# Kernel optimization log

Measured on AMD Instinct MI355X. Metric: run time of the kernel, lower is better.

## Reference

```python
import jax, jax.numpy as jnp
import numpy as np
from itertools import permutations

B, S, D = 1024, 16, 128
G_DIMS = [256, 256]
F_DIMS = [256, 256]

# all ordered pairs (i, j), i != j, in the same lexicographic order as
# itertools.permutations used by the torch module
_PAIRS = np.array(list(permutations(range(S), 2)), dtype=np.int32)  # [P, 2], P = S*(S-1)


def _init_linear(key, in_dim, out_dim):
    kw, kb = jax.random.split(key)
    bound = 1.0 / np.sqrt(in_dim)
    W = jax.random.uniform(kw, (in_dim, out_dim), jnp.float32, -bound, bound)
    b = jax.random.uniform(kb, (out_dim,), jnp.float32, -bound, bound)
    return W, b


def setup_inputs() -> dict:
    key = jax.random.key(0)
    ks = jax.random.split(key, 5)
    state = jax.random.normal(ks[0], (B, S, D), jnp.float32)
    gW0, gb0 = _init_linear(ks[1], 2 * D, G_DIMS[0])
    gW1, gb1 = _init_linear(ks[2], G_DIMS[0], G_DIMS[1])
    fW0, fb0 = _init_linear(ks[3], G_DIMS[1], F_DIMS[0])
    fW1, fb1 = _init_linear(ks[4], F_DIMS[0], F_DIMS[1])
    return {"state": state,
            "gW0": gW0, "gb0": gb0, "gW1": gW1, "gb1": gb1,
            "fW0": fW0, "fb0": fb0, "fW1": fW1, "fb1": fb1}


def reference(state, gW0, gb0, gW1, gb1, fW0, fb0, fW1, fb1):
    i_idx = jnp.asarray(_PAIRS[:, 0])
    j_idx = jnp.asarray(_PAIRS[:, 1])
    # gather + concat all ordered pairs: [B, P, 2D]
    paired = jnp.concatenate([state[:, i_idx], state[:, j_idx]], axis=-1)
    # g-MLP applied per pair
    h = jax.nn.relu(jnp.einsum('bpd,de->bpe', paired, gW0) + gb0)
    h = jax.nn.relu(jnp.einsum('bpd,de->bpe', h, gW1) + gb1)
    # sum over pairs -> [B, g_out]
    pooled = h.sum(axis=1)
    # f-MLP
    out = jax.nn.relu(pooled @ fW0 + fb0)
    out = jax.nn.relu(out @ fW1 + fb1)
    return out
```

## Files before the change

### kernel.cpp

```cpp
#include <hip/hip_runtime.h>

typedef __attribute__((ext_vector_type(8))) _Float16 f16x8;
typedef __attribute__((ext_vector_type(4))) float f32x4;

#define HSTR 264

__global__ __launch_bounds__(256) void prep_kernel(
    const float* __restrict__ gW0, const float* __restrict__ gW1,
    _Float16* __restrict__ W0c, _Float16* __restrict__ W1c)
{
  const int t = blockIdx.x * 256 + threadIdx.x;
  {
    const int c = t >> 7, k = t & 127;
    const int dst = ((k >> 5) * 32 + (c >> 4)) * 512 +
                    (((k >> 3) & 3) * 16 + (c & 15)) * 8 + (k & 7);
    const int src = (k + ((c >= 256) ? 128 : 0)) * 256 + (c & 255);
    W0c[dst] = (_Float16)gW0[src];
  }
  {
    const int n = t >> 8, k = t & 255;
    const int dst = ((k >> 5) * 16 + (n >> 4)) * 512 +
                    (((k >> 3) & 3) * 16 + (n & 15)) * 8 + (k & 7);
    W1c[dst] = (_Float16)gW1[k * 256 + n];
  }
}

__global__ __launch_bounds__(512, 4) void pair_kernel(
    const float* __restrict__ state,
    const _Float16* __restrict__ W0c, const float* __restrict__ gb0,
    const _Float16* __restrict__ W1c, const float* __restrict__ gb1,
    float* __restrict__ pooled)
{
  const int b   = blockIdx.x;
  const int tid = threadIdx.x;
  const int w   = tid >> 6;
  const int l   = tid & 63;
  const int lr  = l & 15;
  const int lg  = l >> 4;

  __shared__ _Float16 A_lds[16 * HSTR];
  __shared__ _Float16 C_lds[16 * HSTR];

  const float* stb = state + (size_t)b * 2048;

  f16x8 sfrag[4];
  #pragma unroll
  for (int kk = 0; kk < 4; ++kk) {
    const float* sp = stb + lr * 128 + kk * 32 + lg * 8;
    f32x4 s0 = *(const f32x4*)sp;
    f32x4 s1 = *(const f32x4*)(sp + 4);
    f16x8 f;
    f[0] = (_Float16)s0[0]; f[1] = (_Float16)s0[1];
    f[2] = (_Float16)s0[2]; f[3] = (_Float16)s0[3];
    f[4] = (_Float16)s1[0]; f[5] = (_Float16)s1[1];
    f[6] = (_Float16)s1[2]; f[7] = (_Float16)s1[3];
    sfrag[kk] = f;
  }

  const f32x4 z4 = {0.f, 0.f, 0.f, 0.f};
  f32x4 acc2[4];
  #pragma unroll
  for (int nt = 0; nt < 4; ++nt) acc2[nt] = z4;

  #pragma unroll
  for (int nt = 0; nt < 4; ++nt) {
    #pragma unroll
    for (int kk = 0; kk < 4; ++kk) {
      f16x8 bf = *(const f16x8*)(W0c + (size_t)((kk * 32 + 4 * w + nt) * 512 + l * 8));
      acc2[nt] = __builtin_amdgcn_mfma_f32_16x16x32_f16(sfrag[kk], bf, acc2[nt], 0, 0, 0);
    }
  }

  #pragma unroll
  for (int nt = 0; nt < 4; ++nt) {
    const int col = 64 * w + 16 * nt + lr;
    #pragma unroll
    for (int r = 0; r < 4; ++r) {
      const int row = lg * 4 + r;
      const float v = acc2[nt][r];
      if (col < 256) A_lds[row * HSTR + col]       = (_Float16)(v + gb0[col]);
      else           C_lds[row * HSTR + col - 256] = (_Float16)v;
    }
  }

  f16x8 bw[2][8];
  #pragma unroll
  for (int nt = 0; nt < 2; ++nt) {
    #pragma unroll
    for (int kk = 0; kk < 8; ++kk) {
      bw[nt][kk] = *(const f16x8*)(W1c + (size_t)((kk * 16 + 2 * w + nt) * 512 + l * 8));
      asm volatile("" : "+a"(bw[nt][kk]));
    }
  }

  float gb1v[2];
  #pragma unroll
  for (int nt = 0; nt < 2; ++nt) gb1v[nt] = gb1[32 * w + 16 * nt + lr];

  __syncthreads();

  f16x8 creg[8];
  #pragma unroll
  for (int kk = 0; kk < 8; ++kk)
    creg[kk] = *(const f16x8*)&C_lds[lr * HSTR + kk * 32 + lg * 8];

  const f16x8 zh = {(_Float16)0, (_Float16)0, (_Float16)0, (_Float16)0,
                    (_Float16)0, (_Float16)0, (_Float16)0, (_Float16)0};

  float pp[2] = {0.f, 0.f};
  #pragma unroll 1
  for (int i = 0; i < 16; ++i) {
    f32x4 a0 = z4, a1 = z4;
    #pragma unroll
    for (int kk = 0; kk < 8; ++kk) {
      f16x8 av = *(const f16x8*)&A_lds[i * HSTR + kk * 32 + lg * 8];
      f16x8 u = __builtin_elementwise_max(av + creg[kk], zh);
      asm volatile("s_nop 3\n\tv_mfma_f32_16x16x32_f16 %0, %1, %2, %0"
                   : "+v"(a0) : "v"(u), "a"(bw[0][kk]));
      asm volatile("v_mfma_f32_16x16x32_f16 %0, %1, %2, %0"
                   : "+v"(a1) : "v"(u), "a"(bw[1][kk]));
    }
    asm volatile("s_nop 7\n\ts_nop 7");

    #pragma unroll
    for (int r = 0; r < 4; ++r) {
      const int row = lg * 4 + r;
      const float v0 = fmaxf(a0[r] + gb1v[0], 0.f);
      const float v1 = fmaxf(a1[r] + gb1v[1], 0.f);
      pp[0] += (row == i) ? 0.f : v0;
      pp[1] += (row == i) ? 0.f : v1;
    }
  }

  #pragma unroll
  for (int nt = 0; nt < 2; ++nt) {
    float v = pp[nt];
    v += __shfl_xor(v, 16);
    v += __shfl_xor(v, 32);
    if (lg == 0) pooled[(size_t)b * 256 + 32 * w + 16 * nt + lr] = v;
  }
}

__global__ __launch_bounds__(256) void fmlp_kernel(
    const float* __restrict__ pooled,
    const float* __restrict__ fW0, const float* __restrict__ fb0,
    const float* __restrict__ fW1, const float* __restrict__ fb1,
    float* __restrict__ out)
{
  const int tid = threadIdx.x;
  const size_t b0 = (size_t)blockIdx.x * 4;
  __shared__ float pl[4][256];
  __shared__ float h1[4][256];

  #pragma unroll
  for (int q = 0; q < 4; ++q)
    pl[q][tid] = pooled[(b0 + q) * 256 + tid];
  __syncthreads();

  float acc[4] = {0.f, 0.f, 0.f, 0.f};
  #pragma unroll 8
  for (int k = 0; k < 256; ++k) {
    const float wv = fW0[(size_t)k * 256 + tid];
    #pragma unroll
    for (int q = 0; q < 4; ++q) acc[q] = fmaf(pl[q][k], wv, acc[q]);
  }
  #pragma unroll
  for (int q = 0; q < 4; ++q) h1[q][tid] = fmaxf(acc[q] + fb0[tid], 0.f);
  __syncthreads();

  float acc2[4] = {0.f, 0.f, 0.f, 0.f};
  #pragma unroll 8
  for (int k = 0; k < 256; ++k) {
    const float wv = fW1[(size_t)k * 256 + tid];
    #pragma unroll
    for (int q = 0; q < 4; ++q) acc2[q] = fmaf(h1[q][k], wv, acc2[q]);
  }
  #pragma unroll
  for (int q = 0; q < 4; ++q)
    out[(b0 + q) * 256 + tid] = fmaxf(acc2[q] + fb1[tid], 0.f);
}

extern "C" void kernel_launch(void* const* d_in, const int* in_sizes, int n_in,
                              void* d_out, int out_size, void* d_ws, size_t ws_size,
                              hipStream_t stream) {
  const float* state = (const float*)d_in[0];
  const float* gW0   = (const float*)d_in[1];
  const float* gb0   = (const float*)d_in[2];
  const float* gW1   = (const float*)d_in[3];
  const float* gb1   = (const float*)d_in[4];
  const float* fW0   = (const float*)d_in[5];
  const float* fb0   = (const float*)d_in[6];
  const float* fW1   = (const float*)d_in[7];
  const float* fb1   = (const float*)d_in[8];
  float* out = (float*)d_out;

  _Float16* W0c = (_Float16*)d_ws;
  _Float16* W1c = W0c + 65536;
  float* pooled = (float*)(W1c + 65536);

  const int Bn = in_sizes[0] / 2048;

  prep_kernel<<<dim3(256), dim3(256), 0, stream>>>(gW0, gW1, W0c, W1c);
  pair_kernel<<<dim3(Bn), dim3(512), 0, stream>>>(state, W0c, gb0, W1c, gb1, pooled);
  fmlp_kernel<<<dim3(Bn / 4), dim3(256), 0, stream>>>(pooled, fW0, fb0, fW1, fb1, out);
}
```

Baseline: 73.95 us.

## Share ReLU-combined pair inputs across warps via swizzled LDS buffers

Previously every warp computed relu(A_i + C) for all 16 i and all 8 k-chunks on its own, repeating the same elementwise work 8 times across warps. Now each warp computes a quarter of the k-chunks for one i per group of four. It writes the fp16 results into an XOR-swizzled LDS tile, and all warps then read those shared tiles as MFMA A operands. This cuts redundant VALU add/max work and register use for C fragments. In exchange it adds LDS round trips, 8 extra block barriers, and more shared memory per block, which may lower occupancy.

Result: faster. 71.50 us (-3.3%).

```diff
diff --git a/kernel.cpp b/kernel.cpp
--- a/kernel.cpp
+++ b/kernel.cpp
@@ -38,8 +38,10 @@
   const int lr  = l & 15;
   const int lg  = l >> 4;
 
-  __shared__ _Float16 A_lds[16 * HSTR];
-  __shared__ _Float16 C_lds[16 * HSTR];
+  __shared__ __align__(16) char smem[8448 + 32768];
+  _Float16* A_lds = (_Float16*)smem;
+  char*     ubuf  = smem + 8448;
+  _Float16* C_st  = (_Float16*)ubuf;
 
   const float* stb = state + (size_t)b * 2048;
 
@@ -71,6 +73,19 @@
     }
   }
 
+  f16x8 bw[2][8];
+  #pragma unroll
+  for (int nt = 0; nt < 2; ++nt) {
+    #pragma unroll
+    for (int kk = 0; kk < 8; ++kk) {
+      bw[nt][kk] = *(const f16x8*)(W1c + (size_t)((kk * 16 + 2 * w + nt) * 512 + l * 8));
+      asm volatile("" : "+a"(bw[nt][kk]));
+    }
+  }
+  float gb1v[2];
+  gb1v[0] = gb1[32 * w + lr];
+  gb1v[1] = gb1[32 * w + 16 + lr];
+
   #pragma unroll
   for (int nt = 0; nt < 4; ++nt) {
     const int col = 64 * w + 16 * nt + lr;
@@ -79,65 +94,82 @@
       const int row = lg * 4 + r;
       const float v = acc2[nt][r];
       if (col < 256) A_lds[row * HSTR + col]       = (_Float16)(v + gb0[col]);
-      else           C_lds[row * HSTR + col - 256] = (_Float16)v;
-    }
-  }
-
-  f16x8 bw[2][8];
-  #pragma unroll
-  for (int nt = 0; nt < 2; ++nt) {
-    #pragma unroll
-    for (int kk = 0; kk < 8; ++kk) {
-      bw[nt][kk] = *(const f16x8*)(W1c + (size_t)((kk * 16 + 2 * w + nt) * 512 + l * 8));
-      asm volatile("" : "+a"(bw[nt][kk]));
-    }
-  }
-
-  float gb1v[2];
-  #pragma unroll
-  for (int nt = 0; nt < 2; ++nt) gb1v[nt] = gb1[32 * w + 16 * nt + lr];
-
-  __syncthreads();
-
-  f16x8 creg[8];
-  #pragma unroll
-  for (int kk = 0; kk < 8; ++kk)
-    creg[kk] = *(const f16x8*)&C_lds[lr * HSTR + kk * 32 + lg * 8];
+      else           C_st[row * HSTR + col - 256]  = (_Float16)v;
+    }
+  }
+  __syncthreads();
+
+  const int kh = (w & 1) * 4;
+  f16x8 creg[4];
+  #pragma unroll
+  for (int kq = 0; kq < 4; ++kq)
+    creg[kq] = *(const f16x8*)&C_st[lr * HSTR + (kh + kq) * 32 + lg * 8];
+  __syncthreads();
+
+  const int lrd = (lr * 64 + lg * 16) ^ ((lr & 7) << 4);
 
   const f16x8 zh = {(_Float16)0, (_Float16)0, (_Float16)0, (_Float16)0,
                     (_Float16)0, (_Float16)0, (_Float16)0, (_Float16)0};
 
-  float pp[2] = {0.f, 0.f};
+  float pp0 = 0.f, pp1 = 0.f;
+
   #pragma unroll 1
-  for (int i = 0; i < 16; ++i) {
-    f32x4 a0 = z4, a1 = z4;
-    #pragma unroll
-    for (int kk = 0; kk < 8; ++kk) {
-      f16x8 av = *(const f16x8*)&A_lds[i * HSTR + kk * 32 + lg * 8];
-      f16x8 u = __builtin_elementwise_max(av + creg[kk], zh);
-      asm volatile("s_nop 3\n\tv_mfma_f32_16x16x32_f16 %0, %1, %2, %0"
-                   : "+v"(a0) : "v"(u), "a"(bw[0][kk]));
-      asm volatile("v_mfma_f32_16x16x32_f16 %0, %1, %2, %0"
-                   : "+v"(a1) : "v"(u), "a"(bw[1][kk]));
-    }
-    asm volatile("s_nop 7\n\ts_nop 7");
-
-    #pragma unroll
-    for (int r = 0; r < 4; ++r) {
-      const int row = lg * 4 + r;
-      const float v0 = fmaxf(a0[r] + gb1v[0], 0.f);
-      const float v1 = fmaxf(a1[r] + gb1v[1], 0.f);
-      pp[0] += (row == i) ? 0.f : v0;
-      pp[1] += (row == i) ? 0.f : v1;
-    }
-  }
-
-  #pragma unroll
-  for (int nt = 0; nt < 2; ++nt) {
-    float v = pp[nt];
+  for (int g = 0; g < 4; ++g) {
+    {
+      const int ip = 4 * g + (w >> 1);
+      char* tb = ubuf + (w >> 1) * 8192;
+      #pragma unroll
+      for (int kq = 0; kq < 4; ++kq) {
+        const int kk = kh + kq;
+        f16x8 av = *(const f16x8*)&A_lds[ip * HSTR + kk * 32 + lg * 8];
+        f16x8 u = __builtin_elementwise_max(av + creg[kq], zh);
+        *(f16x8*)(tb + kk * 1024 + lrd) = u;
+      }
+    }
+    __syncthreads();
+
+    #pragma unroll
+    for (int t = 0; t < 4; ++t) {
+      const char* tb = ubuf + t * 8192;
+      f32x4 a0 = z4, a1 = z4;
+      #pragma unroll
+      for (int kk = 0; kk < 8; ++kk) {
+        f16x8 uf = *(const f16x8*)(tb + kk * 1024 + lrd);
+        if (kk == 0)
+          asm volatile("s_nop 3\n\tv_mfma_f32_16x16x32_f16 %0, %1, %2, %0"
+                       : "+v"(a0) : "v"(uf), "a"(bw[0][kk]));
+        else
+          asm volatile("v_mfma_f32_16x16x32_f16 %0, %1, %2, %0"
+                       : "+v"(a0) : "v"(uf), "a"(bw[0][kk]));
+        asm volatile("v_mfma_f32_16x16x32_f16 %0, %1, %2, %0"
+                     : "+v"(a1) : "v"(uf), "a"(bw[1][kk]));
+      }
+      asm volatile("s_nop 7\n\ts_nop 7");
+
+      const int i = 4 * g + t;
+      #pragma unroll
+      for (int r = 0; r < 4; ++r) {
+        const int row = lg * 4 + r;
+        const float v0 = fmaxf(a0[r] + gb1v[0], 0.f);
+        const float v1 = fmaxf(a1[r] + gb1v[1], 0.f);
+        pp0 += (row == i) ? 0.f : v0;
+        pp1 += (row == i) ? 0.f : v1;
+      }
+    }
+    __syncthreads();
+  }
+
+  {
+    float v = pp0;
     v += __shfl_xor(v, 16);
     v += __shfl_xor(v, 32);
-    if (lg == 0) pooled[(size_t)b * 256 + 32 * w + 16 * nt + lr] = v;
+    if (lg == 0) pooled[(size_t)b * 256 + 32 * w + lr] = v;
+  }
+  {
+    float v = pp1;
+    v += __shfl_xor(v, 16);
+    v += __shfl_xor(v, 32);
+    if (lg == 0) pooled[(size_t)b * 256 + 32 * w + 16 + lr] = v;
   }
 }
 
```

## Precompute relu pair inputs into LDS and retile layer-2 MFMA work across waves

Applied to the files above, without the earlier changes.

Each wave now builds the relu(A_i + C_j) fp16 fragments for two pair-rows i and stores all 16 of them in a 128KB LDS buffer. Layer 2 is then retiled so each wave covers 64 output columns (4 N-tiles, 32 weight fragments held in AGPRs) for 8 of the i values. Partial sums from the two i-halves are reduced through LDS before the global write. This drops the hand-scheduled asm MFMA with s_nop padding and the per-wave recomputation of the elementwise prep, and gives each A fragment load 4 MFMAs instead of 2. The cost is roughly 140KB of LDS per block, which limits occupancy to about one block per CU (launch bound lowered to 2), plus extra barriers.

Measured after the change: 91.95 us. 24.3% more time.

```diff
diff --git a/kernel.cpp b/kernel.cpp
--- a/kernel.cpp
+++ b/kernel.cpp
@@ -25,7 +25,7 @@
   }
 }
 
-__global__ __launch_bounds__(512, 4) void pair_kernel(
+__global__ __launch_bounds__(512, 2) void pair_kernel(
     const float* __restrict__ state,
     const _Float16* __restrict__ W0c, const float* __restrict__ gb0,
     const _Float16* __restrict__ W1c, const float* __restrict__ gb1,
@@ -38,8 +38,10 @@
   const int lr  = l & 15;
   const int lg  = l >> 4;
 
-  __shared__ _Float16 A_lds[16 * HSTR];
-  __shared__ _Float16 C_lds[16 * HSTR];
+  __shared__ __align__(16) char smem[8448 + 131072];
+  _Float16* A_lds = (_Float16*)smem;
+  char*     ubuf  = smem + 8448;
+  _Float16* C_st  = (_Float16*)ubuf;
 
   const float* stb = state + (size_t)b * 2048;
 
@@ -71,6 +73,20 @@
     }
   }
 
+  const int n4 = w & 3;
+  f16x8 bw[4][8];
+  #pragma unroll
+  for (int nt = 0; nt < 4; ++nt) {
+    #pragma unroll
+    for (int kk = 0; kk < 8; ++kk) {
+      bw[nt][kk] = *(const f16x8*)(W1c + (size_t)((kk * 16 + 4 * n4 + nt) * 512 + l * 8));
+      asm volatile("" : "+a"(bw[nt][kk]));
+    }
+  }
+  float gb1v[4];
+  #pragma unroll
+  for (int nt = 0; nt < 4; ++nt) gb1v[nt] = gb1[64 * n4 + 16 * nt + lr];
+
   #pragma unroll
   for (int nt = 0; nt < 4; ++nt) {
     const int col = 64 * w + 16 * nt + lr;
@@ -79,66 +95,72 @@
       const int row = lg * 4 + r;
       const float v = acc2[nt][r];
       if (col < 256) A_lds[row * HSTR + col]       = (_Float16)(v + gb0[col]);
-      else           C_lds[row * HSTR + col - 256] = (_Float16)v;
-    }
-  }
-
-  f16x8 bw[2][8];
-  #pragma unroll
-  for (int nt = 0; nt < 2; ++nt) {
-    #pragma unroll
-    for (int kk = 0; kk < 8; ++kk) {
-      bw[nt][kk] = *(const f16x8*)(W1c + (size_t)((kk * 16 + 2 * w + nt) * 512 + l * 8));
-      asm volatile("" : "+a"(bw[nt][kk]));
-    }
-  }
-
-  float gb1v[2];
-  #pragma unroll
-  for (int nt = 0; nt < 2; ++nt) gb1v[nt] = gb1[32 * w + 16 * nt + lr];
-
+      else           C_st[row * HSTR + col - 256]  = (_Float16)v;
+    }
+  }
   __syncthreads();
 
   f16x8 creg[8];
   #pragma unroll
   for (int kk = 0; kk < 8; ++kk)
-    creg[kk] = *(const f16x8*)&C_lds[lr * HSTR + kk * 32 + lg * 8];
+    creg[kk] = *(const f16x8*)&C_st[lr * HSTR + kk * 32 + lg * 8];
+  __syncthreads();
 
   const f16x8 zh = {(_Float16)0, (_Float16)0, (_Float16)0, (_Float16)0,
                     (_Float16)0, (_Float16)0, (_Float16)0, (_Float16)0};
 
-  float pp[2] = {0.f, 0.f};
-  #pragma unroll 1
-  for (int i = 0; i < 16; ++i) {
-    f32x4 a0 = z4, a1 = z4;
+  #pragma unroll
+  for (int tt = 0; tt < 2; ++tt) {
+    const int ip = 2 * w + tt;
+    char* tb = ubuf + ip * 8192;
     #pragma unroll
     for (int kk = 0; kk < 8; ++kk) {
-      f16x8 av = *(const f16x8*)&A_lds[i * HSTR + kk * 32 + lg * 8];
+      f16x8 av = *(const f16x8*)&A_lds[ip * HSTR + kk * 32 + lg * 8];
       f16x8 u = __builtin_elementwise_max(av + creg[kk], zh);
-      asm volatile("s_nop 3\n\tv_mfma_f32_16x16x32_f16 %0, %1, %2, %0"
-                   : "+v"(a0) : "v"(u), "a"(bw[0][kk]));
-      asm volatile("v_mfma_f32_16x16x32_f16 %0, %1, %2, %0"
-                   : "+v"(a1) : "v"(u), "a"(bw[1][kk]));
-    }
-    asm volatile("s_nop 7\n\ts_nop 7");
-
-    #pragma unroll
-    for (int r = 0; r < 4; ++r) {
-      const int row = lg * 4 + r;
-      const float v0 = fmaxf(a0[r] + gb1v[0], 0.f);
-      const float v1 = fmaxf(a1[r] + gb1v[1], 0.f);
-      pp[0] += (row == i) ? 0.f : v0;
-      pp[1] += (row == i) ? 0.f : v1;
-    }
-  }
-
-  #pragma unroll
-  for (int nt = 0; nt < 2; ++nt) {
+      *(f16x8*)(tb + kk * 1024 + l * 16) = u;
+    }
+  }
+  __syncthreads();
+
+  const int mg = w >> 2;
+  float pp[4] = {0.f, 0.f, 0.f, 0.f};
+  #pragma unroll 2
+  for (int t8 = 0; t8 < 8; ++t8) {
+    const int i = 8 * mg + t8;
+    const char* tb = ubuf + i * 8192;
+    f32x4 acc[4];
+    #pragma unroll
+    for (int nt = 0; nt < 4; ++nt) acc[nt] = z4;
+    #pragma unroll
+    for (int kk = 0; kk < 8; ++kk) {
+      f16x8 uf = *(const f16x8*)(tb + kk * 1024 + l * 16);
+      #pragma unroll
+      for (int nt = 0; nt < 4; ++nt)
+        acc[nt] = __builtin_amdgcn_mfma_f32_16x16x32_f16(uf, bw[nt][kk], acc[nt], 0, 0, 0);
+    }
+    #pragma unroll
+    for (int nt = 0; nt < 4; ++nt) {
+      #pragma unroll
+      for (int r = 0; r < 4; ++r) {
+        const int row = lg * 4 + r;
+        const float v = fmaxf(acc[nt][r] + gb1v[nt], 0.f);
+        pp[nt] += (row == i) ? 0.f : v;
+      }
+    }
+  }
+  __syncthreads();
+
+  float* pool = (float*)ubuf;
+  #pragma unroll
+  for (int nt = 0; nt < 4; ++nt) {
     float v = pp[nt];
     v += __shfl_xor(v, 16);
     v += __shfl_xor(v, 32);
-    if (lg == 0) pooled[(size_t)b * 256 + 32 * w + 16 * nt + lr] = v;
-  }
+    if (lg == 0) pool[mg * 256 + 64 * n4 + 16 * nt + lr] = v;
+  }
+  __syncthreads();
+  if (tid < 256)
+    pooled[(size_t)b * 256 + tid] = pool[tid] + pool[256 + tid];
 }
 
 __global__ __launch_bounds__(256) void fmlp_kernel(
```
